# Optimization experiments

Measured on AMD Instinct MI355X. Metric: run time of the kernel, lower is better.

## Reference

```python
import jax, jax.numpy as jnp
import numpy as np

B, T, E, H, D, NL = 2, 1024, 2048, 16, 128, 3
MAXL = T * (2 ** (NL - 1))  # k length doubles each layer: T, 2T, 4T


def _rms_norm(x, w, eps=1e-5):
    return x * jax.lax.rsqrt(jnp.mean(x * x, axis=-1, keepdims=True) + eps) * w


def _rope(x, cos, sin):
    # x: [B, S, H, D]; cos/sin: [>=S, D/2]; GPT-NeoX style (non-interleaved)
    S = x.shape[1]
    c = cos[:S][None, :, None, :]
    s = sin[:S][None, :, None, :]
    x1, x2 = jnp.split(x, 2, axis=-1)
    return jnp.concatenate([x1 * c - x2 * s, x1 * s + x2 * c], axis=-1)


def _causal_attn(q, k, v):
    # bottom-right-aligned causal (flash_attn_func causal=True with kv longer than q)
    Tq, L = q.shape[1], k.shape[1]
    scale = 1.0 / np.sqrt(q.shape[-1]).astype(np.float32)
    scores = jnp.einsum('bthd,bshd->bhts', q, k) * scale
    i = jnp.arange(Tq)[:, None]
    j = jnp.arange(L)[None, :]
    mask = j <= i + (L - Tq)
    scores = jnp.where(mask[None, None], scores, -jnp.inf)
    p = jax.nn.softmax(scores, axis=-1)
    return jnp.einsum('bhts,bshd->bthd', p, v)


def setup_inputs() -> dict:
    key = jax.random.key(0)
    ks = jax.random.split(key, 6)
    x = jax.random.normal(ks[0], (B, T, E), dtype=jnp.float32)
    inv_freq = 1.0 / (10000.0 ** (np.arange(0, D, 2, dtype=np.float32) / D))  # [D/2]
    ang = np.arange(MAXL, dtype=np.float32)[:, None] * inv_freq[None, :]      # [MAXL, D/2]
    cos = jnp.asarray(np.cos(ang), dtype=jnp.float32)
    sin = jnp.asarray(np.sin(ang), dtype=jnp.float32)
    wq = jax.random.normal(ks[1], (NL, E, E), dtype=jnp.float32) * 0.02
    wk = jax.random.normal(ks[2], (NL, E, E), dtype=jnp.float32) * 0.02
    wv = jax.random.normal(ks[3], (NL, E, E), dtype=jnp.float32) * 0.02
    ln_w = jnp.ones((NL, E), dtype=jnp.float32)
    lambdas = jnp.zeros((NL,), dtype=jnp.float32)
    w_out = jax.random.normal(ks[4], (E, E), dtype=jnp.float32) * 0.02
    final_ln_w = jnp.ones((E,), dtype=jnp.float32)
    alpha = jnp.ones((1,), dtype=jnp.float32)
    return {'x': x, 'cos': cos, 'sin': sin, 'wq': wq, 'wk': wk, 'wv': wv,
            'ln_w': ln_w, 'lambdas': lambdas, 'w_out': w_out,
            'final_ln_w': final_ln_w, 'alpha': alpha}


def reference(x, cos, sin, wq, wk, wv, ln_w, lambdas, w_out, final_ln_w, alpha):
    bsz, tgt_len, embed_dim = x.shape
    # lambda weights: sigmoid then LayerNorm over the NL scalars (no affine)
    lam = jax.nn.sigmoid(lambdas)
    lam = (lam - jnp.mean(lam)) * jax.lax.rsqrt(jnp.var(lam) + 1e-5)
    acc_k, acc_v = [], []
    total = jnp.zeros_like(x)
    for i in range(NL):  # small fixed layer count
        q = (x @ wq[i].T).reshape(bsz, tgt_len, H, D)
        k = (x @ wk[i].T).reshape(bsz, tgt_len, H, D)
        v = (x @ wv[i].T).reshape(bsz, tgt_len, H, D)
        if i > 0:
            k = jnp.concatenate([k] + acc_k, axis=1)
            v = jnp.concatenate([v] + acc_v, axis=1)
        q = _rope(q, cos, sin)
        k = _rope(k, cos, sin)  # note: cached K gets rotary re-applied, as in source
        attn = _causal_attn(q, k, v).reshape(bsz, tgt_len, embed_dim)
        attn = _rms_norm(attn, ln_w[i])
        total = total + attn * lam[i]
        acc_k.append(k)
        acc_v.append(v)
    out = _rms_norm(total + alpha * x, final_ln_w)
    return out @ w_out.T
```

## Files before the change

### kernel.cpp

```cpp
#include <hip/hip_runtime.h>

typedef unsigned short ushort_t;
typedef __attribute__((ext_vector_type(8))) short bf16x8;
typedef __attribute__((ext_vector_type(4))) short bf16x4;
typedef __attribute__((ext_vector_type(4))) float f32x4;
typedef __attribute__((ext_vector_type(4))) unsigned short u16x4;
typedef __attribute__((ext_vector_type(4))) unsigned int u32x4;

#define DEV __device__ __forceinline__

DEV ushort_t f2bf(float f) {
  union { float f; unsigned int u; } a; a.f = f;
  unsigned int u = a.u;
  unsigned int r = (u + 0x7fffu + ((u >> 16) & 1u)) >> 16;
  return (ushort_t)r;
}
DEV float bf2f(ushort_t b) {
  union { float f; unsigned int u; } a; a.u = ((unsigned int)b) << 16;
  return a.f;
}
DEV void gload_lds16(const void* g, void* l) {
  __builtin_amdgcn_global_load_lds((const __attribute__((address_space(1))) void*)g,
                                   (__attribute__((address_space(3))) void*)l, 16, 0, 0);
}
DEV bf16x4 tr16(const ushort_t* l) {
  unsigned a = (unsigned)(unsigned long long)(const __attribute__((address_space(3))) ushort_t*)l;
  bf16x4 d;
  asm volatile("ds_read_b64_tr_b16 %0, %1" : "=v"(d) : "v"(a));
  return d;
}
DEV bf16x8 ldsb128(const ushort_t* l) {
  unsigned a = (unsigned)(unsigned long long)(const __attribute__((address_space(3))) ushort_t*)l;
  bf16x8 d;
  asm volatile("ds_read_b128 %0, %1" : "=v"(d) : "v"(a));
  return d;
}

__global__ __launch_bounds__(256) void f2b_kernel(const float* __restrict__ in,
                                                  ushort_t* __restrict__ out, int n) {
  int base = (blockIdx.x * 256 + threadIdx.x) * 4;
  if (base >= n) return;
  f32x4 v = *(const f32x4*)(in + base);
  u16x4 o;
  o.x = f2bf(v.x); o.y = f2bf(v.y); o.z = f2bf(v.z); o.w = f2bf(v.w);
  *(u16x4*)(out + base) = o;
}

__global__ __launch_bounds__(256) void f2b3_kernel(const float* __restrict__ a, const float* __restrict__ b,
                                                   const float* __restrict__ c, ushort_t* __restrict__ out) {
  int id = blockIdx.x * 256 + threadIdx.x;
  int sel = id >> 20, k = (id & 1048575) * 4;
  const float* src = sel == 0 ? a : sel == 1 ? b : c;
  f32x4 v = *(const f32x4*)(src + k);
  u16x4 o;
  o.x = f2bf(v.x); o.y = f2bf(v.y); o.z = f2bf(v.z); o.w = f2bf(v.w);
  *(u16x4*)(out + (size_t)sel * 4194304 + k) = o;
}

__global__ void lam_kernel(const float* __restrict__ lambdas, float* __restrict__ lam) {
  if (threadIdx.x == 0 && blockIdx.x == 0) {
    float l0 = 1.f / (1.f + __expf(-lambdas[0]));
    float l1 = 1.f / (1.f + __expf(-lambdas[1]));
    float l2 = 1.f / (1.f + __expf(-lambdas[2]));
    float mean = (l0 + l1 + l2) * (1.f / 3.f);
    float d0 = l0 - mean, d1 = l1 - mean, d2 = l2 - mean;
    float var = (d0 * d0 + d1 * d1 + d2 * d2) * (1.f / 3.f);
    float rs = rsqrtf(var + 1e-5f);
    lam[0] = d0 * rs; lam[1] = d1 * rs; lam[2] = d2 * rs;
  }
}

DEV void gemm_core(const ushort_t* __restrict__ A, const ushort_t* __restrict__ Bm,
                   ushort_t* lsA, ushort_t* lsB, int bm, int bn, f32x4 (&acc)[4][4]) {
  const int K = 2048;
  int tid = threadIdx.x;
  int w = tid >> 6, lane = tid & 63;
  int g = lane >> 4, r = lane & 15;
  int wm = w >> 1, wn = w & 1;
#pragma unroll
  for (int i = 0; i < 4; ++i)
#pragma unroll
    for (int j = 0; j < 4; ++j) acc[i][j] = 0.f;

  for (int kk = 0; kk < K; kk += 32) {
    __syncthreads();
#pragma unroll
    for (int j2 = 0; j2 < 2; ++j2) {
      int eb = w * 1024 + j2 * 512;
      int ebl = eb + lane * 8;
      int rr = ebl >> 5, cc = ebl & 31;
      gload_lds16(A + (size_t)(bm * 128 + rr) * K + kk + cc, lsA + eb);
      gload_lds16(Bm + (size_t)(bn * 128 + rr) * K + kk + cc, lsB + eb);
    }
    __syncthreads();
    bf16x8 af[4], bfr[4];
#pragma unroll
    for (int i = 0; i < 4; ++i)
      af[i] = *(const bf16x8*)(lsA + (wm * 64 + i * 16 + r) * 32 + g * 8);
#pragma unroll
    for (int j = 0; j < 4; ++j)
      bfr[j] = *(const bf16x8*)(lsB + (wn * 64 + j * 16 + r) * 32 + g * 8);
#pragma unroll
    for (int i = 0; i < 4; ++i)
#pragma unroll
      for (int j = 0; j < 4; ++j)
        acc[i][j] = __builtin_amdgcn_mfma_f32_16x16x32_bf16(af[i], bfr[j], acc[i][j], 0, 0, 0);
  }
}

__global__ __launch_bounds__(256) void gemm_qkv(
    const ushort_t* __restrict__ A,
    const ushort_t* __restrict__ Bq, const ushort_t* __restrict__ Bk, const ushort_t* __restrict__ Bv,
    ushort_t* __restrict__ Cq, ushort_t* __restrict__ Ck, ushort_t* __restrict__ Cv, int Lkv) {
  __shared__ __align__(16) ushort_t lsA[4096];
  __shared__ __align__(16) ushort_t lsB[4096];
  int sel = blockIdx.x >> 4, bn = blockIdx.x & 15, bm = blockIdx.y;
  const ushort_t* Bm = (sel == 0) ? Bq : (sel == 1) ? Bk : Bv;
  ushort_t* C = (sel == 0) ? Cq : (sel == 1) ? Ck : Cv;
  int Lsel = (sel == 0) ? 1024 : Lkv;
  f32x4 acc[4][4];
  gemm_core(A, Bm, lsA, lsB, bm, bn, acc);
  int lane = threadIdx.x & 63, w = threadIdx.x >> 6;
  int g = lane >> 4, r = lane & 15, wm = w >> 1, wn = w & 1;
#pragma unroll
  for (int i = 0; i < 4; ++i)
#pragma unroll
    for (int j = 0; j < 4; ++j) {
      int row0 = bm * 128 + wm * 64 + i * 16 + g * 4;
      int col = bn * 128 + wn * 64 + j * 16 + r;
#pragma unroll
      for (int t = 0; t < 4; ++t) {
        int row = row0 + t;
        int b2 = row >> 10, t2 = row & 1023;
        C[(size_t)(b2 * Lsel + t2) * 2048 + col] = f2bf(acc[i][j][t]);
      }
    }
}

__global__ __launch_bounds__(256) void gemm_bt_f32(
    const ushort_t* __restrict__ A, const ushort_t* __restrict__ Bm, float* __restrict__ C) {
  __shared__ __align__(16) ushort_t lsA[4096];
  __shared__ __align__(16) ushort_t lsB[4096];
  int bn = blockIdx.x, bm = blockIdx.y;
  f32x4 acc[4][4];
  gemm_core(A, Bm, lsA, lsB, bm, bn, acc);
  int lane = threadIdx.x & 63, w = threadIdx.x >> 6;
  int g = lane >> 4, r = lane & 15, wm = w >> 1, wn = w & 1;
#pragma unroll
  for (int i = 0; i < 4; ++i)
#pragma unroll
    for (int j = 0; j < 4; ++j) {
      int row0 = bm * 128 + wm * 64 + i * 16 + g * 4;
      int col = bn * 128 + wn * 64 + j * 16 + r;
#pragma unroll
      for (int t = 0; t < 4; ++t)
        C[(size_t)(row0 + t) * 2048 + col] = acc[i][j][t];
    }
}

__global__ __launch_bounds__(256) void rope_seg(const ushort_t* __restrict__ src, ushort_t* __restrict__ dst,
                                                const float* __restrict__ cosT, const float* __restrict__ sinT,
                                                int Ls, int s0, int Ld, int dpos0, int cnt) {
  int bp = blockIdx.x;
  int b = bp / cnt, pidx = bp % cnt;
  int pos = dpos0 + pidx;
  int pi = threadIdx.x * 4;
  int h = pi >> 6, d = pi & 63;
  const ushort_t* s_ = src + ((size_t)(b * Ls + s0 + pidx) * 16 + h) * 128 + d;
  ushort_t* d_ = dst + ((size_t)(b * Ld + pos) * 16 + h) * 128 + d;
  f32x4 c4 = *(const f32x4*)(cosT + (size_t)pos * 64 + d);
  f32x4 s4 = *(const f32x4*)(sinT + (size_t)pos * 64 + d);
  u16x4 x1 = *(const u16x4*)(s_);
  u16x4 x2 = *(const u16x4*)(s_ + 64);
  u16x4 o1, o2;
#pragma unroll
  for (int k = 0; k < 4; ++k) {
    float a = bf2f(x1[k]), bb = bf2f(x2[k]);
    o1[k] = f2bf(a * c4[k] - bb * s4[k]);
    o2[k] = f2bf(a * s4[k] + bb * c4[k]);
  }
  *(u16x4*)d_ = o1;
  *(u16x4*)(d_ + 64) = o2;
}

__global__ __launch_bounds__(256) void copy_seg(const ushort_t* __restrict__ src, ushort_t* __restrict__ dst,
                                                int Ls, int s0, int Ld, int dpos0, int cnt) {
  int bp = blockIdx.x;
  int b = bp / cnt, pidx = bp % cnt;
  const u32x4* s = (const u32x4*)(src + (size_t)(b * Ls + s0 + pidx) * 2048);
  u32x4* d = (u32x4*)(dst + (size_t)(b * Ld + dpos0 + pidx) * 2048);
  d[threadIdx.x] = s[threadIdx.x];
}

__global__ __launch_bounds__(256) void attn_kernel(
    const ushort_t* __restrict__ Q, const ushort_t* __restrict__ Kc, const ushort_t* __restrict__ Vc,
    float* __restrict__ Oout, int Lk) {
  __shared__ __align__(16) ushort_t lsK[8192];
  __shared__ __align__(16) ushort_t lsV[8192];
  const float sc = 0.08838834764831843f;

  int bid = (int)blockIdx.x;
  int swz = (bid & 7) * 64 + (bid >> 3);

  int w = threadIdx.x >> 6, lane = threadIdx.x & 63;
  int wid = swz * 4 + w;
  int qt = wid & 63, h = (wid >> 6) & 15, b = wid >> 10;
  int bq = swz & 15;
  int g = lane >> 4, r = lane & 15;
  int off = Lk - 1024;

  const ushort_t* qbase = Q + ((size_t)(b * 1024 + qt * 16 + r) * 16 + h) * 128;
  bf16x8 qf[4];
#pragma unroll
  for (int c = 0; c < 4; ++c) qf[c] = *(const bf16x8*)(qbase + c * 32 + g * 8);

  int t = threadIdx.x;
  int krow0 = t >> 4,        kc0 = (t & 15) ^ (krow0 & 7);
  int krow1 = (t + 256) >> 4, kc1 = (t & 15) ^ (krow1 & 7);
  const ushort_t* srcK0 = Kc + ((size_t)(b * Lk + krow0) * 16 + h) * 128 + kc0 * 8;
  const ushort_t* srcK1 = Kc + ((size_t)(b * Lk + krow1) * 16 + h) * 128 + kc1 * 8;
  int L0 = t, L1 = t + 256;
  int vrow0 = ((L0 >> 3) & 7) * 4 + ((L0 >> 1) & 3), vd0 = (L0 >> 6) * 16 + (L0 & 1) * 8;
  int vrow1 = ((L1 >> 3) & 7) * 4 + ((L1 >> 1) & 3), vd1 = (L1 >> 6) * 16 + (L1 & 1) * 8;
  const ushort_t* srcV0 = Vc + ((size_t)(b * Lk + vrow0) * 16 + h) * 128 + vd0;
  const ushort_t* srcV1 = Vc + ((size_t)(b * Lk + vrow1) * 16 + h) * 128 + vd1;
  const size_t adv = 32 * 2048;

  auto STAGE = [&](int buf) {
    ushort_t* k0 = lsK + buf * 4096 + w * 512;
    ushort_t* v0 = lsV + buf * 4096 + w * 512;
    gload_lds16(srcK0, k0);
    gload_lds16(srcK1, k0 + 2048);
    gload_lds16(srcV0, v0);
    gload_lds16(srcV1, v0 + 2048);
    srcK0 += adv; srcK1 += adv; srcV0 += adv; srcV1 += adv;
  };

  float m_run = -1e30f, l_run = 0.f;
  f32x4 o[8];
#pragma unroll
  for (int c = 0; c < 8; ++c) o[c] = 0.f;

  int qp = qt * 16 + r + off;
  int nkt_w = ((qt * 16 + 15 + off) >> 5) + 1;
  int nkt_blk = (((bq * 4 + 3) * 16 + 15 + off) >> 5) + 1;

  STAGE(0);

  for (int kt = 0; kt < nkt_blk; ++kt) {
    int cur = kt & 1;
    if (kt + 1 < nkt_blk) {
      STAGE(cur ^ 1);
      asm volatile("s_waitcnt vmcnt(4)" ::: "memory");
    } else {
      asm volatile("s_waitcnt vmcnt(0)" ::: "memory");
    }
    __builtin_amdgcn_s_barrier();
    __builtin_amdgcn_sched_barrier(0);
    if (kt < nkt_w) {
      const ushort_t* Kb = lsK + cur * 4096;
      const ushort_t* Vb = lsV + cur * 4096;
      bf16x8 kf[8];
#pragma unroll
      for (int ks = 0; ks < 2; ++ks)
#pragma unroll
        for (int c = 0; c < 4; ++c)
          kf[ks * 4 + c] = ldsb128(Kb + (ks * 16 + r) * 128 + ((c * 32 + g * 8) ^ ((r & 7) * 8)));
      bf16x4 vf[16];
#pragma unroll
      for (int i = 0; i < 16; ++i) vf[i] = tr16(Vb + i * 256);
      asm volatile("s_waitcnt lgkmcnt(15)" ::: "memory");
      __builtin_amdgcn_sched_barrier(0);
      __builtin_amdgcn_s_setprio(1);
      f32x4 st[2];
      st[0] = 0.f; st[1] = 0.f;
#pragma unroll
      for (int ks = 0; ks < 2; ++ks)
#pragma unroll
        for (int c = 0; c < 4; ++c)
          st[ks] = __builtin_amdgcn_mfma_f32_16x16x32_bf16(kf[ks * 4 + c], qf[c], st[ks], 0, 0, 0);
      __builtin_amdgcn_s_setprio(0);
      float pvv[2][4];
      float pmax = -1e30f;
      int kp0 = kt * 32;
#pragma unroll
      for (int ks = 0; ks < 2; ++ks)
#pragma unroll
        for (int j = 0; j < 4; ++j) {
          int key = kp0 + ks * 16 + g * 4 + j;
          float s = st[ks][j] * sc;
          if (key > qp) s = -1e30f;
          pvv[ks][j] = s;
          pmax = fmaxf(pmax, s);
        }
      pmax = fmaxf(pmax, __shfl_xor(pmax, 16, 64));
      pmax = fmaxf(pmax, __shfl_xor(pmax, 32, 64));
      if (!__all(pmax <= m_run + 8.f)) {
        float mnew = fmaxf(m_run, pmax);
        float corr = __expf(m_run - mnew);
        l_run *= corr;
#pragma unroll
        for (int c = 0; c < 8; ++c)
#pragma unroll
          for (int tt = 0; tt < 4; ++tt) o[c][tt] *= corr;
        m_run = mnew;
      }
      float psum = 0.f;
      bf16x4 pf[2];
#pragma unroll
      for (int ks = 0; ks < 2; ++ks)
#pragma unroll
        for (int j = 0; j < 4; ++j) {
          float pe = __expf(pvv[ks][j] - m_run);
          psum += pe;
          pf[ks][j] = (short)f2bf(pe);
        }
      psum += __shfl_xor(psum, 16, 64);
      psum += __shfl_xor(psum, 32, 64);
      l_run += psum;
      asm volatile("s_waitcnt lgkmcnt(0)" ::: "memory");
      __builtin_amdgcn_sched_barrier(0);
      __builtin_amdgcn_s_setprio(1);
#pragma unroll
      for (int dblk = 0; dblk < 8; ++dblk) {
        o[dblk] = __builtin_amdgcn_mfma_f32_16x16x16bf16_1k(vf[dblk * 2], pf[0], o[dblk], 0, 0, 0);
        o[dblk] = __builtin_amdgcn_mfma_f32_16x16x16bf16_1k(vf[dblk * 2 + 1], pf[1], o[dblk], 0, 0, 0);
      }
      __builtin_amdgcn_s_setprio(0);
    }
    __builtin_amdgcn_sched_barrier(0);
    __builtin_amdgcn_s_barrier();
  }
  float linv = 1.f / l_run;
  float* ob = Oout + ((size_t)(b * 1024 + qt * 16 + r) * 16 + h) * 128;
#pragma unroll
  for (int dblk = 0; dblk < 8; ++dblk) {
    f32x4 res;
#pragma unroll
    for (int tt = 0; tt < 4; ++tt) res[tt] = o[dblk][tt] * linv;
    *(f32x4*)(ob + dblk * 16 + g * 4) = res;
  }
}

template <int FIRST>
__global__ __launch_bounds__(256) void rms_accum(const float* __restrict__ attn, const float* __restrict__ lnw,
                                                 const float* __restrict__ lam, int li,
                                                 float* __restrict__ total) {
  int row = blockIdx.x;
  const float* a = attn + (size_t)row * 2048;
  int t8 = threadIdx.x * 8;
  f32x4 v0 = *(const f32x4*)(a + t8);
  f32x4 v1 = *(const f32x4*)(a + t8 + 4);
  float ss = v0.x * v0.x + v0.y * v0.y + v0.z * v0.z + v0.w * v0.w +
             v1.x * v1.x + v1.y * v1.y + v1.z * v1.z + v1.w * v1.w;
#pragma unroll
  for (int m = 1; m < 64; m <<= 1) ss += __shfl_xor(ss, m, 64);
  __shared__ float red[4];
  int w = threadIdx.x >> 6, lane = threadIdx.x & 63;
  if (lane == 0) red[w] = ss;
  __syncthreads();
  ss = red[0] + red[1] + red[2] + red[3];
  float s = rsqrtf(ss * (1.f / 2048.f) + 1e-5f) * lam[li];
  f32x4 w0 = *(const f32x4*)(lnw + t8);
  f32x4 w1 = *(const f32x4*)(lnw + t8 + 4);
  float* o = total + (size_t)row * 2048 + t8;
  f32x4 r0, r1;
#pragma unroll
  for (int k = 0; k < 4; ++k) { r0[k] = v0[k] * s * w0[k]; r1[k] = v1[k] * s * w1[k]; }
  if (!FIRST) {
    f32x4 p0 = *(const f32x4*)(o);
    f32x4 p1 = *(const f32x4*)(o + 4);
#pragma unroll
    for (int k = 0; k < 4; ++k) { r0[k] += p0[k]; r1[k] += p1[k]; }
  }
  *(f32x4*)(o) = r0;
  *(f32x4*)(o + 4) = r1;
}

__global__ __launch_bounds__(256) void final_norm(const float* __restrict__ total, const float* __restrict__ x,
                                                  const float* __restrict__ alphap, const float* __restrict__ flw,
                                                  ushort_t* __restrict__ ybf) {
  int row = blockIdx.x;
  float al = alphap[0];
  int t8 = threadIdx.x * 8;
  const float* tp = total + (size_t)row * 2048 + t8;
  const float* xp = x + (size_t)row * 2048 + t8;
  f32x4 t0 = *(const f32x4*)(tp);
  f32x4 t1 = *(const f32x4*)(tp + 4);
  f32x4 x0 = *(const f32x4*)(xp);
  f32x4 x1 = *(const f32x4*)(xp + 4);
  float y[8];
#pragma unroll
  for (int k = 0; k < 4; ++k) { y[k] = t0[k] + al * x0[k]; y[4 + k] = t1[k] + al * x1[k]; }
  float ss = 0.f;
#pragma unroll
  for (int k = 0; k < 8; ++k) ss += y[k] * y[k];
#pragma unroll
  for (int m = 1; m < 64; m <<= 1) ss += __shfl_xor(ss, m, 64);
  __shared__ float red[4];
  int w = threadIdx.x >> 6, lane = threadIdx.x & 63;
  if (lane == 0) red[w] = ss;
  __syncthreads();
  ss = red[0] + red[1] + red[2] + red[3];
  float s = rsqrtf(ss * (1.f / 2048.f) + 1e-5f);
  f32x4 w0 = *(const f32x4*)(flw + t8);
  f32x4 w1 = *(const f32x4*)(flw + t8 + 4);
  u16x4 o0, o1;
#pragma unroll
  for (int k = 0; k < 4; ++k) {
    o0[k] = f2bf(y[k] * s * w0[k]);
    o1[k] = f2bf(y[4 + k] * s * w1[k]);
  }
  *(u16x4*)(ybf + (size_t)row * 2048 + t8) = o0;
  *(u16x4*)(ybf + (size_t)row * 2048 + t8 + 4) = o1;
}

extern "C" void kernel_launch(void* const* d_in, const int* in_sizes, int n_in,
                              void* d_out, int out_size, void* d_ws, size_t ws_size,
                              hipStream_t stream) {
  const float* x = (const float*)d_in[0];
  const float* cosT = (const float*)d_in[1];
  const float* sinT = (const float*)d_in[2];
  const float* wq = (const float*)d_in[3];
  const float* wk = (const float*)d_in[4];
  const float* wv = (const float*)d_in[5];
  const float* lnw = (const float*)d_in[6];
  const float* lambdas = (const float*)d_in[7];
  const float* w_out = (const float*)d_in[8];
  const float* flw = (const float*)d_in[9];
  const float* alpha = (const float*)d_in[10];

  const size_t ME = 4194304ull;
  char* p = (char*)d_ws;
  size_t off = 0;
  auto alc = [&](size_t bytes) -> void* {
    void* r = p + off;
    off += (bytes + 255) & ~(size_t)255;
    return r;
  };
  ushort_t* xb = (ushort_t*)alc(ME * 2);
  ushort_t* wl = (ushort_t*)alc(3 * ME * 2);
  ushort_t* q = (ushort_t*)alc(ME * 2);
  ushort_t* K0 = (ushort_t*)alc(ME * 2);
  ushort_t* K1 = (ushort_t*)alc(2 * ME * 2);
  ushort_t* K2 = (ushort_t*)alc(4 * ME * 2);
  ushort_t* V0 = (ushort_t*)alc(ME * 2);
  ushort_t* V1 = (ushort_t*)alc(2 * ME * 2);
  ushort_t* V2 = (ushort_t*)alc(4 * ME * 2);
  float* attn = (float*)alc(ME * 4);
  float* total = (float*)alc(ME * 4);
  float* lam = (float*)alc(256);
  ushort_t* ybf = q;

  f2b_kernel<<<4096, 256, 0, stream>>>(x, xb, 4194304);
  lam_kernel<<<1, 64, 0, stream>>>(lambdas, lam);

  ushort_t* Kc[3] = {K0, K1, K2};
  ushort_t* Vc[3] = {V0, V1, V2};

  for (int li = 0; li < 3; ++li) {
    int L = 1024 << li;
    size_t woff = (size_t)li * ME;
    f2b3_kernel<<<12288, 256, 0, stream>>>(wq + woff, wk + woff, wv + woff, wl);
    gemm_qkv<<<dim3(48, 16), 256, 0, stream>>>(xb, wl, wl + ME, wl + 2 * ME,
                                               q, Kc[li], Vc[li], L);
    rope_seg<<<2048, 256, 0, stream>>>(q, q, cosT, sinT, 1024, 0, 1024, 0, 1024);
    rope_seg<<<2048, 256, 0, stream>>>(Kc[li], Kc[li], cosT, sinT, L, 0, L, 0, 1024);
    if (li == 1) {
      rope_seg<<<2048, 256, 0, stream>>>(K0, K1, cosT, sinT, 1024, 0, 2048, 1024, 1024);
      copy_seg<<<2048, 256, 0, stream>>>(V0, V1, 1024, 0, 2048, 1024, 1024);
    } else if (li == 2) {
      copy_seg<<<2048, 256, 0, stream>>>(K1, K2, 2048, 1024, 4096, 1024, 1024);
      rope_seg<<<4096, 256, 0, stream>>>(K1, K2, cosT, sinT, 2048, 0, 4096, 2048, 2048);
      copy_seg<<<2048, 256, 0, stream>>>(V1, V2, 2048, 1024, 4096, 1024, 1024);
      copy_seg<<<4096, 256, 0, stream>>>(V1, V2, 2048, 0, 4096, 2048, 2048);
    }
    attn_kernel<<<512, 256, 0, stream>>>(q, Kc[li], Vc[li], attn, L);
    if (li == 0)
      rms_accum<1><<<2048, 256, 0, stream>>>(attn, lnw, lam, 0, total);
    else
      rms_accum<0><<<2048, 256, 0, stream>>>(attn, lnw + (size_t)li * 2048, lam, li, total);
  }

  f2b_kernel<<<4096, 256, 0, stream>>>(w_out, wl, 4194304);
  final_norm<<<2048, 256, 0, stream>>>(total, x, alpha, flw, ybf);
  gemm_bt_f32<<<dim3(16, 16), 256, 0, stream>>>(ybf, wl, (float*)d_out);
}
```

Before: 636.7 us.

## Split attention KV range across two blocks and combine partials in RMS kernel

The attention kernel now launches twice as many blocks, and each one handles alternating 32-key tiles (split-K flash decoding). It writes unnormalized partial outputs plus per-row max and sum. The RMS-accumulate kernel is turned into a combine kernel that merges the two partials with log-sum-exp weights before normalizing. The aim is more parallelism and better load balance for the causal attention on a 512-block grid. The cost is extra partial-output traffic, which aliases the weight scratch buffer.

```diff
diff --git a/kernel.cpp b/kernel.cpp
--- a/kernel.cpp
+++ b/kernel.cpp
@@ -194,18 +194,19 @@
 
 __global__ __launch_bounds__(256) void attn_kernel(
     const ushort_t* __restrict__ Q, const ushort_t* __restrict__ Kc, const ushort_t* __restrict__ Vc,
-    float* __restrict__ Oout, int Lk) {
+    float* __restrict__ Opart, float2* __restrict__ Ml, int Lk) {
   __shared__ __align__(16) ushort_t lsK[8192];
   __shared__ __align__(16) ushort_t lsV[8192];
   const float sc = 0.08838834764831843f;
 
   int bid = (int)blockIdx.x;
-  int swz = (bid & 7) * 64 + (bid >> 3);
+  int swz = (bid & 7) * 128 + (bid >> 3);
+  int s = swz & 1;
+  int rest = swz >> 1;
 
   int w = threadIdx.x >> 6, lane = threadIdx.x & 63;
-  int wid = swz * 4 + w;
-  int qt = wid & 63, h = (wid >> 6) & 15, b = wid >> 10;
-  int bq = swz & 15;
+  int bq = rest & 15, h = (rest >> 4) & 15, b = rest >> 8;
+  int qt = bq * 4 + w;
   int g = lane >> 4, r = lane & 15;
   int off = Lk - 1024;
 
@@ -217,14 +218,15 @@
   int t = threadIdx.x;
   int krow0 = t >> 4,        kc0 = (t & 15) ^ (krow0 & 7);
   int krow1 = (t + 256) >> 4, kc1 = (t & 15) ^ (krow1 & 7);
-  const ushort_t* srcK0 = Kc + ((size_t)(b * Lk + krow0) * 16 + h) * 128 + kc0 * 8;
-  const ushort_t* srcK1 = Kc + ((size_t)(b * Lk + krow1) * 16 + h) * 128 + kc1 * 8;
+  const size_t adv = 32 * 2048;
+  const size_t adv2 = 2 * adv;
+  const ushort_t* srcK0 = Kc + ((size_t)(b * Lk + krow0) * 16 + h) * 128 + kc0 * 8 + s * adv;
+  const ushort_t* srcK1 = Kc + ((size_t)(b * Lk + krow1) * 16 + h) * 128 + kc1 * 8 + s * adv;
   int L0 = t, L1 = t + 256;
   int vrow0 = ((L0 >> 3) & 7) * 4 + ((L0 >> 1) & 3), vd0 = (L0 >> 6) * 16 + (L0 & 1) * 8;
   int vrow1 = ((L1 >> 3) & 7) * 4 + ((L1 >> 1) & 3), vd1 = (L1 >> 6) * 16 + (L1 & 1) * 8;
-  const ushort_t* srcV0 = Vc + ((size_t)(b * Lk + vrow0) * 16 + h) * 128 + vd0;
-  const ushort_t* srcV1 = Vc + ((size_t)(b * Lk + vrow1) * 16 + h) * 128 + vd1;
-  const size_t adv = 32 * 2048;
+  const ushort_t* srcV0 = Vc + ((size_t)(b * Lk + vrow0) * 16 + h) * 128 + vd0 + s * adv;
+  const ushort_t* srcV1 = Vc + ((size_t)(b * Lk + vrow1) * 16 + h) * 128 + vd1 + s * adv;
 
   auto STAGE = [&](int buf) {
     ushort_t* k0 = lsK + buf * 4096 + w * 512;
@@ -233,7 +235,7 @@
     gload_lds16(srcK1, k0 + 2048);
     gload_lds16(srcV0, v0);
     gload_lds16(srcV1, v0 + 2048);
-    srcK0 += adv; srcK1 += adv; srcV0 += adv; srcV1 += adv;
+    srcK0 += adv2; srcK1 += adv2; srcV0 += adv2; srcV1 += adv2;
   };
 
   float m_run = -1e30f, l_run = 0.f;
@@ -244,113 +246,131 @@
   int qp = qt * 16 + r + off;
   int nkt_w = ((qt * 16 + 15 + off) >> 5) + 1;
   int nkt_blk = (((bq * 4 + 3) * 16 + 15 + off) >> 5) + 1;
-
-  STAGE(0);
-
-  for (int kt = 0; kt < nkt_blk; ++kt) {
-    int cur = kt & 1;
-    if (kt + 1 < nkt_blk) {
-      STAGE(cur ^ 1);
-      asm volatile("s_waitcnt vmcnt(4)" ::: "memory");
-    } else {
-      asm volatile("s_waitcnt vmcnt(0)" ::: "memory");
+  int ntile = (nkt_blk - s + 1) >> 1;
+
+  if (ntile > 0) {
+    STAGE(0);
+    for (int it = 0; it < ntile; ++it) {
+      int kt = s + it * 2;
+      int cur = it & 1;
+      if (it + 1 < ntile) {
+        STAGE(cur ^ 1);
+        asm volatile("s_waitcnt vmcnt(4)" ::: "memory");
+      } else {
+        asm volatile("s_waitcnt vmcnt(0)" ::: "memory");
+      }
+      __builtin_amdgcn_s_barrier();
+      __builtin_amdgcn_sched_barrier(0);
+      if (kt < nkt_w) {
+        const ushort_t* Kb = lsK + cur * 4096;
+        const ushort_t* Vb = lsV + cur * 4096;
+        bf16x8 kf[8];
+#pragma unroll
+        for (int ks = 0; ks < 2; ++ks)
+#pragma unroll
+          for (int c = 0; c < 4; ++c)
+            kf[ks * 4 + c] = ldsb128(Kb + (ks * 16 + r) * 128 + ((c * 32 + g * 8) ^ ((r & 7) * 8)));
+        bf16x4 vf[16];
+#pragma unroll
+        for (int i = 0; i < 16; ++i) vf[i] = tr16(Vb + i * 256);
+        asm volatile("s_waitcnt lgkmcnt(15)" ::: "memory");
+        __builtin_amdgcn_sched_barrier(0);
+        __builtin_amdgcn_s_setprio(1);
+        f32x4 st[2];
+        st[0] = 0.f; st[1] = 0.f;
+#pragma unroll
+        for (int ks = 0; ks < 2; ++ks)
+#pragma unroll
+          for (int c = 0; c < 4; ++c)
+            st[ks] = __builtin_amdgcn_mfma_f32_16x16x32_bf16(kf[ks * 4 + c], qf[c], st[ks], 0, 0, 0);
+        __builtin_amdgcn_s_setprio(0);
+        float pvv[2][4];
+        float pmax = -1e30f;
+        int kp0 = kt * 32;
+#pragma unroll
+        for (int ks = 0; ks < 2; ++ks)
+#pragma unroll
+          for (int j = 0; j < 4; ++j) {
+            int key = kp0 + ks * 16 + g * 4 + j;
+            float sv = st[ks][j] * sc;
+            if (key > qp) sv = -1e30f;
+            pvv[ks][j] = sv;
+            pmax = fmaxf(pmax, sv);
+          }
+        pmax = fmaxf(pmax, __shfl_xor(pmax, 16, 64));
+        pmax = fmaxf(pmax, __shfl_xor(pmax, 32, 64));
+        if (!__all(pmax <= m_run + 8.f)) {
+          float mnew = fmaxf(m_run, pmax);
+          float corr = __expf(m_run - mnew);
+          l_run *= corr;
+#pragma unroll
+          for (int c = 0; c < 8; ++c)
+#pragma unroll
+            for (int tt = 0; tt < 4; ++tt) o[c][tt] *= corr;
+          m_run = mnew;
+        }
+        float psum = 0.f;
+        bf16x4 pf[2];
+#pragma unroll
+        for (int ks = 0; ks < 2; ++ks)
+#pragma unroll
+          for (int j = 0; j < 4; ++j) {
+            float pe = __expf(pvv[ks][j] - m_run);
+            psum += pe;
+            pf[ks][j] = (short)f2bf(pe);
+          }
+        psum += __shfl_xor(psum, 16, 64);
+        psum += __shfl_xor(psum, 32, 64);
+        l_run += psum;
+        asm volatile("s_waitcnt lgkmcnt(0)" ::: "memory");
+        __builtin_amdgcn_sched_barrier(0);
+        __builtin_amdgcn_s_setprio(1);
+#pragma unroll
+        for (int dblk = 0; dblk < 8; ++dblk) {
+          o[dblk] = __builtin_amdgcn_mfma_f32_16x16x16bf16_1k(vf[dblk * 2], pf[0], o[dblk], 0, 0, 0);
+          o[dblk] = __builtin_amdgcn_mfma_f32_16x16x16bf16_1k(vf[dblk * 2 + 1], pf[1], o[dblk], 0, 0, 0);
+        }
+        __builtin_amdgcn_s_setprio(0);
+      }
+      __builtin_amdgcn_sched_barrier(0);
+      __builtin_amdgcn_s_barrier();
     }
-    __builtin_amdgcn_s_barrier();
-    __builtin_amdgcn_sched_barrier(0);
-    if (kt < nkt_w) {
-      const ushort_t* Kb = lsK + cur * 4096;
-      const ushort_t* Vb = lsV + cur * 4096;
-      bf16x8 kf[8];
-#pragma unroll
-      for (int ks = 0; ks < 2; ++ks)
-#pragma unroll
-        for (int c = 0; c < 4; ++c)
-          kf[ks * 4 + c] = ldsb128(Kb + (ks * 16 + r) * 128 + ((c * 32 + g * 8) ^ ((r & 7) * 8)));
-      bf16x4 vf[16];
-#pragma unroll
-      for (int i = 0; i < 16; ++i) vf[i] = tr16(Vb + i * 256);
-      asm volatile("s_waitcnt lgkmcnt(15)" ::: "memory");
-      __builtin_amdgcn_sched_barrier(0);
-      __builtin_amdgcn_s_setprio(1);
-      f32x4 st[2];
-      st[0] = 0.f; st[1] = 0.f;
-#pragma unroll
-      for (int ks = 0; ks < 2; ++ks)
-#pragma unroll
-        for (int c = 0; c < 4; ++c)
-          st[ks] = __builtin_amdgcn_mfma_f32_16x16x32_bf16(kf[ks * 4 + c], qf[c], st[ks], 0, 0, 0);
-      __builtin_amdgcn_s_setprio(0);
-      float pvv[2][4];
-      float pmax = -1e30f;
-      int kp0 = kt * 32;
-#pragma unroll
-      for (int ks = 0; ks < 2; ++ks)
-#pragma unroll
-        for (int j = 0; j < 4; ++j) {
-          int key = kp0 + ks * 16 + g * 4 + j;
-          float s = st[ks][j] * sc;
-          if (key > qp) s = -1e30f;
-          pvv[ks][j] = s;
-          pmax = fmaxf(pmax, s);
-        }
-      pmax = fmaxf(pmax, __shfl_xor(pmax, 16, 64));
-      pmax = fmaxf(pmax, __shfl_xor(pmax, 32, 64));
-      if (!__all(pmax <= m_run + 8.f)) {
-        float mnew = fmaxf(m_run, pmax);
-        float corr = __expf(m_run - mnew);
-        l_run *= corr;
-#pragma unroll
-        for (int c = 0; c < 8; ++c)
-#pragma unroll
-          for (int tt = 0; tt < 4; ++tt) o[c][tt] *= corr;
-        m_run = mnew;
-      }
-      float psum = 0.f;
-      bf16x4 pf[2];
-#pragma unroll
-      for (int ks = 0; ks < 2; ++ks)
-#pragma unroll
-        for (int j = 0; j < 4; ++j) {
-          float pe = __expf(pvv[ks][j] - m_run);
-          psum += pe;
-          pf[ks][j] = (short)f2bf(pe);
-        }
-      psum += __shfl_xor(psum, 16, 64);
-      psum += __shfl_xor(psum, 32, 64);
-      l_run += psum;
-      asm volatile("s_waitcnt lgkmcnt(0)" ::: "memory");
-      __builtin_amdgcn_sched_barrier(0);
-      __builtin_amdgcn_s_setprio(1);
-#pragma unroll
-      for (int dblk = 0; dblk < 8; ++dblk) {
-        o[dblk] = __builtin_amdgcn_mfma_f32_16x16x16bf16_1k(vf[dblk * 2], pf[0], o[dblk], 0, 0, 0);
-        o[dblk] = __builtin_amdgcn_mfma_f32_16x16x16bf16_1k(vf[dblk * 2 + 1], pf[1], o[dblk], 0, 0, 0);
-      }
-      __builtin_amdgcn_s_setprio(0);
-    }
-    __builtin_amdgcn_sched_barrier(0);
-    __builtin_amdgcn_s_barrier();
-  }
-  float linv = 1.f / l_run;
-  float* ob = Oout + ((size_t)(b * 1024 + qt * 16 + r) * 16 + h) * 128;
-#pragma unroll
-  for (int dblk = 0; dblk < 8; ++dblk) {
-    f32x4 res;
-#pragma unroll
-    for (int tt = 0; tt < 4; ++tt) res[tt] = o[dblk][tt] * linv;
-    *(f32x4*)(ob + dblk * 16 + g * 4) = res;
+  }
+  float* ob = Opart + (size_t)s * 4194304 + ((size_t)(b * 1024 + qt * 16 + r) * 16 + h) * 128;
+#pragma unroll
+  for (int dblk = 0; dblk < 8; ++dblk)
+    *(f32x4*)(ob + dblk * 16 + g * 4) = o[dblk];
+  if (g == 0) {
+    float2 ml; ml.x = m_run; ml.y = l_run;
+    Ml[((size_t)(s * 2 + b) * 1024 + qt * 16 + r) * 16 + h] = ml;
   }
 }
 
 template <int FIRST>
-__global__ __launch_bounds__(256) void rms_accum(const float* __restrict__ attn, const float* __restrict__ lnw,
-                                                 const float* __restrict__ lam, int li,
-                                                 float* __restrict__ total) {
+__global__ __launch_bounds__(256) void rms_combine(const float* __restrict__ Opart, const float2* __restrict__ Ml,
+                                                   const float* __restrict__ lnw, const float* __restrict__ lam,
+                                                   int li, float* __restrict__ total) {
   int row = blockIdx.x;
-  const float* a = attn + (size_t)row * 2048;
   int t8 = threadIdx.x * 8;
-  f32x4 v0 = *(const f32x4*)(a + t8);
-  f32x4 v1 = *(const f32x4*)(a + t8 + 4);
+  int h = t8 >> 7;
+  float2 ml0 = Ml[(size_t)row * 16 + h];
+  float2 ml1 = Ml[(size_t)(row + 2048) * 16 + h];
+  float M = fmaxf(ml0.x, ml1.x);
+  float w0 = __expf(ml0.x - M), w1 = __expf(ml1.x - M);
+  float rinv = 1.f / (w0 * ml0.y + w1 * ml1.y);
+  w0 *= rinv; w1 *= rinv;
+  const float* a0 = Opart + (size_t)row * 2048 + t8;
+  const float* a1 = a0 + 4194304;
+  f32x4 p00 = *(const f32x4*)(a0);
+  f32x4 p01 = *(const f32x4*)(a0 + 4);
+  f32x4 p10 = *(const f32x4*)(a1);
+  f32x4 p11 = *(const f32x4*)(a1 + 4);
+  f32x4 v0, v1;
+#pragma unroll
+  for (int k = 0; k < 4; ++k) {
+    v0[k] = w0 * p00[k] + w1 * p10[k];
+    v1[k] = w0 * p01[k] + w1 * p11[k];
+  }
   float ss = v0.x * v0.x + v0.y * v0.y + v0.z * v0.z + v0.w * v0.w +
              v1.x * v1.x + v1.y * v1.y + v1.z * v1.z + v1.w * v1.w;
 #pragma unroll
@@ -360,18 +380,18 @@
   if (lane == 0) red[w] = ss;
   __syncthreads();
   ss = red[0] + red[1] + red[2] + red[3];
-  float s = rsqrtf(ss * (1.f / 2048.f) + 1e-5f) * lam[li];
-  f32x4 w0 = *(const f32x4*)(lnw + t8);
-  f32x4 w1 = *(const f32x4*)(lnw + t8 + 4);
+  float sca = rsqrtf(ss * (1.f / 2048.f) + 1e-5f) * lam[li];
+  f32x4 w0v = *(const f32x4*)(lnw + t8);
+  f32x4 w1v = *(const f32x4*)(lnw + t8 + 4);
   float* o = total + (size_t)row * 2048 + t8;
   f32x4 r0, r1;
 #pragma unroll
-  for (int k = 0; k < 4; ++k) { r0[k] = v0[k] * s * w0[k]; r1[k] = v1[k] * s * w1[k]; }
+  for (int k = 0; k < 4; ++k) { r0[k] = v0[k] * sca * w0v[k]; r1[k] = v1[k] * sca * w1v[k]; }
   if (!FIRST) {
-    f32x4 p0 = *(const f32x4*)(o);
-    f32x4 p1 = *(const f32x4*)(o + 4);
-#pragma unroll
-    for (int k = 0; k < 4; ++k) { r0[k] += p0[k]; r1[k] += p1[k]; }
+    f32x4 q0 = *(const f32x4*)(o);
+    f32x4 q1 = *(const f32x4*)(o + 4);
+#pragma unroll
+    for (int k = 0; k < 4; ++k) { r0[k] += q0[k]; r1[k] += q1[k]; }
   }
   *(f32x4*)(o) = r0;
   *(f32x4*)(o + 4) = r1;
@@ -439,7 +459,9 @@
     return r;
   };
   ushort_t* xb = (ushort_t*)alc(ME * 2);
-  ushort_t* wl = (ushort_t*)alc(3 * ME * 2);
+  void* uni = alc(2 * ME * 4);
+  ushort_t* wl = (ushort_t*)uni;
+  float* Opart = (float*)uni;
   ushort_t* q = (ushort_t*)alc(ME * 2);
   ushort_t* K0 = (ushort_t*)alc(ME * 2);
   ushort_t* K1 = (ushort_t*)alc(2 * ME * 2);
@@ -447,8 +469,8 @@
   ushort_t* V0 = (ushort_t*)alc(ME * 2);
   ushort_t* V1 = (ushort_t*)alc(2 * ME * 2);
   ushort_t* V2 = (ushort_t*)alc(4 * ME * 2);
-  float* attn = (float*)alc(ME * 4);
   float* total = (float*)alc(ME * 4);
+  float2* Ml = (float2*)alc(65536 * 8);
   float* lam = (float*)alc(256);
   ushort_t* ybf = q;
 
@@ -475,11 +497,11 @@
       copy_seg<<<2048, 256, 0, stream>>>(V1, V2, 2048, 1024, 4096, 1024, 1024);
       copy_seg<<<4096, 256, 0, stream>>>(V1, V2, 2048, 0, 4096, 2048, 2048);
     }
-    attn_kernel<<<512, 256, 0, stream>>>(q, Kc[li], Vc[li], attn, L);
+    attn_kernel<<<1024, 256, 0, stream>>>(q, Kc[li], Vc[li], Opart, Ml, L);
     if (li == 0)
-      rms_accum<1><<<2048, 256, 0, stream>>>(attn, lnw, lam, 0, total);
+      rms_combine<1><<<2048, 256, 0, stream>>>(Opart, Ml, lnw, lam, 0, total);
     else
-      rms_accum<0><<<2048, 256, 0, stream>>>(attn, lnw + (size_t)li * 2048, lam, li, total);
+      rms_combine<0><<<2048, 256, 0, stream>>>(Opart, Ml, lnw + (size_t)li * 2048, lam, li, total);
   }
 
   f2b_kernel<<<4096, 256, 0, stream>>>(w_out, wl, 4194304);
```

After: 637.9 us. About the same (+0.2%).
